# Optimization experiments

Measured on AMD Instinct MI355X. Metric: run time of the kernel, lower is better.

The kernel has to match this reference:

```python
import jax, jax.numpy as jnp
import numpy as np

DIM = 512
HEADS = 16
WS = (4, 8, 8)           # window size (z, y, x)
B = 128                  # batch * num_windows
CPB_HIDDEN = 512


def _rel_tables(ws):
    # Faithful to the torch buffers, including the original's use of ws[0]-1
    # as the normalizer for ALL three coordinate channels.
    wz, wy, wx = ws
    lz, ly, lx = 2 * wz - 1, 2 * wy - 1, 2 * wx - 1
    g = np.stack(np.meshgrid(np.arange(lz), np.arange(ly), np.arange(lx), indexing='ij'), 0).astype(np.float32)
    for i in range(3):
        g[i] = (g[i] - (wz - 1)) / (wz - 1)
    table = np.transpose(g, (1, 2, 3, 0)) * 8.0                      # [lz,ly,lx,3]
    table = np.sign(table) * np.log2(np.abs(table) + 1.0) / np.log2(8.0)
    c = np.stack(np.meshgrid(np.arange(wz), np.arange(wy), np.arange(wx), indexing='ij'), 0).reshape(3, -1)
    rel = np.transpose(c[:, :, None] - c[:, None, :], (1, 2, 0))      # [S,S,3]
    rel[:, :, 0] += wz - 1
    rel[:, :, 1] += wy - 1
    rel[:, :, 2] += wx - 1
    idx = rel[:, :, 0] * ly * lx + rel[:, :, 1] * lx + rel[:, :, 2]   # [S,S]
    return table.astype(np.float32), idx.reshape(-1).astype(np.int32)


def setup_inputs() -> dict:
    key = jax.random.key(0)
    ks = jax.random.split(key, 8)
    table, idx = _rel_tables(WS)
    return {
        'hidden_states': jax.random.normal(ks[0], (B, WS[0], WS[1], WS[2], DIM), dtype=jnp.float32),
        'Wqkv': jax.random.normal(ks[1], (3 * DIM, DIM), dtype=jnp.float32) * 0.02,
        'bqkv': jnp.zeros((3 * DIM,), dtype=jnp.float32),
        'Wproj': jax.random.normal(ks[2], (DIM, DIM), dtype=jnp.float32) * 0.02,
        'bproj': jnp.zeros((DIM,), dtype=jnp.float32),
        'logit_scale': jnp.log(10.0 * jnp.ones((HEADS, 1, 1), dtype=jnp.float32)),
        'cpb_w1': jax.random.normal(ks[3], (CPB_HIDDEN, 3), dtype=jnp.float32) * 0.02,
        'cpb_b1': jnp.zeros((CPB_HIDDEN,), dtype=jnp.float32),
        'cpb_w2': jax.random.normal(ks[4], (HEADS, CPB_HIDDEN), dtype=jnp.float32) * 0.02,
        'coords_table': jnp.asarray(table),
        'rel_index': jnp.asarray(idx),
    }


def reference(hidden_states, Wqkv, bqkv, Wproj, bproj, logit_scale,
              cpb_w1, cpb_b1, cpb_w2, coords_table, rel_index):
    b, nz, ny, nx, dim = hidden_states.shape
    H = logit_scale.shape[0]
    d = dim // H
    S = nz * ny * nx

    # qkv projection, split into per-head q/k/v: [b,H,S,d]
    qkv = hidden_states @ Wqkv.T + bqkv            # [b,nz,ny,nx,3*dim]
    qkv = qkv.reshape(b, S, 3, H, d)
    q = jnp.transpose(qkv[:, :, 0], (0, 2, 1, 3))
    k = jnp.transpose(qkv[:, :, 1], (0, 2, 1, 3))
    v = jnp.transpose(qkv[:, :, 2], (0, 2, 1, 3))

    # cosine attention: L2-normalize q,k (eps=1e-12 like F.normalize), learned clamped scale
    scale = jnp.exp(jnp.minimum(logit_scale, jnp.log(100.0)))   # [H,1,1], max 1/0.01
    qn = q / jnp.maximum(jnp.linalg.norm(q, axis=-1, keepdims=True), 1e-12)
    kn = k / jnp.maximum(jnp.linalg.norm(k, axis=-1, keepdims=True), 1e-12)
    qn = qn * scale                                              # broadcast over [b,H,S,d]

    # continuous relative position bias: MLP(coords_table) gathered by rel_index
    bias_table = jax.nn.relu(coords_table @ cpb_w1.T + cpb_b1) @ cpb_w2.T   # [lz,ly,lx,H]
    bias = bias_table.reshape(-1, H)[rel_index].reshape(S, S, H)
    bias = 16.0 * jax.nn.sigmoid(jnp.transpose(bias, (2, 0, 1)))            # [H,S,S]

    attn = jnp.einsum('bhid,bhjd->bhij', qn, kn) + bias[None]
    attn = jax.nn.softmax(attn, axis=-1)
    ctx = jnp.einsum('bhij,bhjd->bhid', attn, v)                            # [b,H,S,d]
    ctx = jnp.transpose(ctx, (0, 2, 1, 3)).reshape(b, nz, ny, nx, dim)
    return ctx @ Wproj.T + bproj
```

## Files before the change

### kernel.cpp

```cpp
#include <hip/hip_runtime.h>
#include <hip/hip_bf16.h>

typedef __bf16 bf16x8 __attribute__((ext_vector_type(8)));
typedef float  f32x4  __attribute__((ext_vector_type(4)));

#define MFMA_BF16 __builtin_amdgcn_mfma_f32_16x16x32_bf16

static __device__ __forceinline__ bf16x8 pack8(float4 a, float4 b) {
    bf16x8 r;
    r[0] = (__bf16)a.x; r[1] = (__bf16)a.y; r[2] = (__bf16)a.z; r[3] = (__bf16)a.w;
    r[4] = (__bf16)b.x; r[5] = (__bf16)b.y; r[6] = (__bf16)b.z; r[7] = (__bf16)b.w;
    return r;
}

static __device__ __forceinline__ void gload16(const void* g, void* l) {
    __builtin_amdgcn_global_load_lds(
        (const __attribute__((address_space(1))) unsigned int*)g,
        (__attribute__((address_space(3))) unsigned int*)l,
        16, 0, 0);
}

__global__ __launch_bounds__(256) void cvt_bf16_kernel(
    const float* __restrict__ src, __bf16* __restrict__ dst)
{
    const size_t i = ((size_t)blockIdx.x * 256 + threadIdx.x) * 8;
    float4 a = *(const float4*)(src + i);
    float4 b = *(const float4*)(src + i + 4);
    *(bf16x8*)(dst + i) = pack8(a, b);
}

__global__ __launch_bounds__(256) void qkv_kernel(
    const __bf16* __restrict__ hsb, const __bf16* __restrict__ Wqb,
    const float* __restrict__ bqkv, const float* __restrict__ lsc,
    __bf16* __restrict__ qn, __bf16* __restrict__ kn, __bf16* __restrict__ vv)
{
    __shared__ __align__(16) __bf16 As[128][64];
    __shared__ __align__(16) __bf16 Bs[128][64];

    const int t = threadIdx.x;
    const int nBase = blockIdx.x * 128;
    const int mBase = blockIdx.y * 128;
    const int wave = t >> 6, lane = t & 63;
    const int wr = wave >> 1, wc = wave & 1;
    const int lhi = lane >> 4, llo = lane & 15;
    const int srow = t >> 3;
    const int scol = (t & 7) * 8;

    const __bf16* gA = hsb + (size_t)(mBase + srow) * 512 + scol;
    const __bf16* gB = Wqb + (size_t)(nBase + srow) * 512 + scol;
    char* lA = (char*)(&As[0][0]) + wave * 1024;
    char* lB = (char*)(&Bs[0][0]) + wave * 1024;

    f32x4 acc[4][4] = {};

    for (int k0 = 0; k0 < 512; k0 += 64) {
        __syncthreads();
        #pragma unroll
        for (int i = 0; i < 4; ++i) {
            gload16(gA + k0 + i * 16384, lA + i * 4096);
            gload16(gB + k0 + i * 16384, lB + i * 4096);
        }
        __syncthreads();
        #pragma unroll
        for (int kk = 0; kk < 64; kk += 32) {
            bf16x8 af[4], bg[4];
            #pragma unroll
            for (int x = 0; x < 4; ++x) {
                af[x] = *(const bf16x8*)&As[wr*64 + x*16 + llo][kk + lhi*8];
                bg[x] = *(const bf16x8*)&Bs[wc*64 + x*16 + llo][kk + lhi*8];
            }
            #pragma unroll
            for (int mi = 0; mi < 4; ++mi)
                #pragma unroll
                for (int ni = 0; ni < 4; ++ni)
                    acc[mi][ni] = MFMA_BF16(af[mi], bg[ni], acc[mi][ni], 0, 0, 0);
        }
    }

    const int nW = nBase + wc * 64;
    const int which = nW >> 9;
    __bf16* outp = (which == 0) ? qn : (which == 1) ? kn : vv;
    float bq[4];
    #pragma unroll
    for (int ni = 0; ni < 4; ++ni) bq[ni] = bqkv[nW + ni*16 + llo];

    #pragma unroll
    for (int p = 0; p < 2; ++p) {
        const int h = ((nW + p*32) >> 5) & 15;
        const float sc = (which == 0) ? __expf(fminf(lsc[h], 4.6051701859880914f))
                                      : 1.0f;
        #pragma unroll
        for (int mi = 0; mi < 4; ++mi) {
            #pragma unroll
            for (int r = 0; r < 4; ++r) {
                float v0 = acc[mi][2*p][r]   + bq[2*p];
                float v1 = acc[mi][2*p+1][r] + bq[2*p+1];
                float f = 1.0f;
                if (which < 2) {
                    float ss = v0*v0 + v1*v1;
                    ss += __shfl_xor(ss, 1);
                    ss += __shfl_xor(ss, 2);
                    ss += __shfl_xor(ss, 4);
                    ss += __shfl_xor(ss, 8);
                    f = sc / fmaxf(sqrtf(ss), 1e-12f);
                }
                const int row = mBase + wr*64 + mi*16 + lhi*4 + r;
                const int b = row >> 8, s = row & 255;
                __bf16* dst = outp + (((size_t)(b*16 + h))*256 + s)*32;
                dst[llo]      = (__bf16)(v0 * f);
                dst[16 + llo] = (__bf16)(v1 * f);
            }
        }
    }
}

__global__ __launch_bounds__(256) void cpb_table_kernel(
    const float* __restrict__ w1, const float* __restrict__ b1,
    const float* __restrict__ w2, const float* __restrict__ coords,
    float* __restrict__ bias_table)
{
    __shared__ float hid[512];
    __shared__ float part[16][17];
    const int e = blockIdx.x;
    const float x = coords[e*3+0], y = coords[e*3+1], z = coords[e*3+2];
    const int t = threadIdx.x;
    for (int c = t; c < 512; c += 256) {
        float v = w1[c*3+0]*x + w1[c*3+1]*y + w1[c*3+2]*z + b1[c];
        hid[c] = fmaxf(v, 0.f);
    }
    __syncthreads();
    const int hh = t >> 4, seg = t & 15;
    float p = 0.f;
    #pragma unroll
    for (int j = 0; j < 32; ++j) p += w2[hh*512 + seg*32 + j] * hid[seg*32 + j];
    part[hh][seg] = p;
    __syncthreads();
    if (t < 16) {
        float s = 0.f;
        #pragma unroll
        for (int i = 0; i < 16; ++i) s += part[t][i];
        bias_table[e*16 + t] = s;
    }
}

__global__ __launch_bounds__(256) void bias_gather_kernel(
    const float* __restrict__ bias_table, const int* __restrict__ rel_index,
    float* __restrict__ bias_f)
{
    const int tid = blockIdx.x * 256 + threadIdx.x;
    const int lane = tid & 63;
    const int j16 = (tid >> 6) & 15;
    const int i16 = (tid >> 10) & 15;
    const int h   = tid >> 14;
    const int llo = lane & 15, lhi = lane >> 4;
    const int qrow = i16*16 + llo;
    float4 o;
    #pragma unroll
    for (int r = 0; r < 4; ++r) {
        int kcol = j16*16 + lhi*4 + r;
        int idx = rel_index[qrow*256 + kcol];
        float v = bias_table[idx*16 + h];
        (&o.x)[r] = 16.f / (1.f + __expf(-v)) - 26.0f;
    }
    ((float4*)bias_f)[tid] = o;
}

__global__ __launch_bounds__(256) void attn_kernel(
    const __bf16* __restrict__ qn, const __bf16* __restrict__ kn,
    const __bf16* __restrict__ vv, const float* __restrict__ bias_f,
    __bf16* __restrict__ ctx)
{
    __shared__ __align__(16) __bf16 Kl[256][40];
    __shared__ __align__(16) __bf16 Vt[32][264];

    const int bh = blockIdx.x;
    const int b = bh >> 4, h = bh & 15;
    const int t = threadIdx.x;
    const int wave = t >> 6, lane = t & 63;
    const int lhi = lane >> 4, llo = lane & 15;
    const size_t base = (size_t)bh * 8192;

    {
        const __bf16* sk = kn + base + t*32;
        #pragma unroll
        for (int j = 0; j < 4; ++j)
            *(bf16x8*)&Kl[t][j*8] = *(const bf16x8*)(sk + j*8);

        const int u = t & 31;
        const int slot = (t & ~31) + 8*((u & 15) >> 2) + (u & 3) + ((u >> 4) & 1)*4;
        const __bf16* sv = vv + base + t*32;
        #pragma unroll
        for (int j = 0; j < 4; ++j) {
            bf16x8 v8 = *(const bf16x8*)(sv + j*8);
            #pragma unroll
            for (int e = 0; e < 8; ++e) Vt[j*8 + e][slot] = v8[e];
        }
    }
    __syncthreads();

    const f32x4* bp4 = (const f32x4*)bias_f + (size_t)h * 16384;

    #pragma unroll 1
    for (int qt = 0; qt < 4; ++qt) {
        const int i16 = wave*4 + qt;
        const int row0 = i16*16;
        bf16x8 bq = *(const bf16x8*)(qn + base + (size_t)(row0 + llo)*32 + lhi*8);

        f32x4 o0 = {0.f,0.f,0.f,0.f}, o1 = {0.f,0.f,0.f,0.f};
        float sum = 0.f;

        #pragma unroll 2
        for (int c = 0; c < 8; ++c) {
            f32x4 bfA = bp4[((size_t)i16*16 + 2*c    )*64 + lane];
            f32x4 bfB = bp4[((size_t)i16*16 + 2*c + 1)*64 + lane];

            bf16x8 ka0 = *(const bf16x8*)&Kl[c*32 + llo][lhi*8];
            bf16x8 ka1 = *(const bf16x8*)&Kl[c*32 + 16 + llo][lhi*8];

            __builtin_amdgcn_s_setprio(1);
            f32x4 stA = MFMA_BF16(ka0, bq, bfA, 0, 0, 0);
            f32x4 stB = MFMA_BF16(ka1, bq, bfB, 0, 0, 0);
            __builtin_amdgcn_s_setprio(0);

            bf16x8 pa;
            #pragma unroll
            for (int r = 0; r < 4; ++r) {
                float eA = __expf(stA[r]);
                float eB = __expf(stB[r]);
                sum += eA + eB;
                pa[r]     = (__bf16)eA;
                pa[r + 4] = (__bf16)eB;
            }

            bf16x8 bv0 = *(const bf16x8*)&Vt[llo][c*32 + lhi*8];
            bf16x8 bv1 = *(const bf16x8*)&Vt[16 + llo][c*32 + lhi*8];

            __builtin_amdgcn_s_setprio(1);
            o0 = MFMA_BF16(pa, bv0, o0, 0, 0, 0);
            o1 = MFMA_BF16(pa, bv1, o1, 0, 0, 0);
            __builtin_amdgcn_s_setprio(0);
        }

        sum += __shfl_xor(sum, 16);
        sum += __shfl_xor(sum, 32);

        #pragma unroll
        for (int r = 0; r < 4; ++r) {
            float inv = __builtin_amdgcn_rcpf(__shfl(sum, lhi*4 + r));
            int srow = row0 + lhi*4 + r;
            __bf16* cp = ctx + ((size_t)(b*256 + srow))*512 + h*32;
            cp[llo]      = (__bf16)(o0[r] * inv);
            cp[16 + llo] = (__bf16)(o1[r] * inv);
        }
    }
}

__global__ __launch_bounds__(256) void proj_kernel(
    const __bf16* __restrict__ ctx, const __bf16* __restrict__ Wpb,
    const float* __restrict__ bpr, float* __restrict__ out)
{
    __shared__ __align__(16) __bf16 As[128][64];
    __shared__ __align__(16) __bf16 Bs[128][64];

    const int t = threadIdx.x;
    const int nBase = blockIdx.x * 128;
    const int mBase = blockIdx.y * 128;
    const int wave = t >> 6, lane = t & 63;
    const int wr = wave >> 1, wc = wave & 1;
    const int lhi = lane >> 4, llo = lane & 15;
    const int srow = t >> 3;
    const int scol = (t & 7) * 8;

    const __bf16* gA = ctx + (size_t)(mBase + srow) * 512 + scol;
    const __bf16* gB = Wpb + (size_t)(nBase + srow) * 512 + scol;
    char* lA = (char*)(&As[0][0]) + wave * 1024;
    char* lB = (char*)(&Bs[0][0]) + wave * 1024;

    f32x4 acc[4][4] = {};

    for (int k0 = 0; k0 < 512; k0 += 64) {
        __syncthreads();
        #pragma unroll
        for (int i = 0; i < 4; ++i) {
            gload16(gA + k0 + i * 16384, lA + i * 4096);
            gload16(gB + k0 + i * 16384, lB + i * 4096);
        }
        __syncthreads();
        #pragma unroll
        for (int kk = 0; kk < 64; kk += 32) {
            bf16x8 af[4], bg[4];
            #pragma unroll
            for (int x = 0; x < 4; ++x) {
                af[x] = *(const bf16x8*)&As[wr*64 + x*16 + llo][kk + lhi*8];
                bg[x] = *(const bf16x8*)&Bs[wc*64 + x*16 + llo][kk + lhi*8];
            }
            #pragma unroll
            for (int mi = 0; mi < 4; ++mi)
                #pragma unroll
                for (int ni = 0; ni < 4; ++ni)
                    acc[mi][ni] = MFMA_BF16(af[mi], bg[ni], acc[mi][ni], 0, 0, 0);
        }
    }

    float bn[4];
    #pragma unroll
    for (int ni = 0; ni < 4; ++ni) bn[ni] = bpr[nBase + wc*64 + ni*16 + llo];

    #pragma unroll
    for (int mi = 0; mi < 4; ++mi)
        #pragma unroll
        for (int ni = 0; ni < 4; ++ni)
            #pragma unroll
            for (int r = 0; r < 4; ++r)
                out[(size_t)(mBase + wr*64 + mi*16 + lhi*4 + r)*512
                    + nBase + wc*64 + ni*16 + llo] = acc[mi][ni][r] + bn[ni];
}

extern "C" void kernel_launch(void* const* d_in, const int* in_sizes, int n_in,
                              void* d_out, int out_size, void* d_ws, size_t ws_size,
                              hipStream_t stream) {
    const float* hs     = (const float*)d_in[0];
    const float* Wqkv   = (const float*)d_in[1];
    const float* bqkv   = (const float*)d_in[2];
    const float* Wproj  = (const float*)d_in[3];
    const float* bproj  = (const float*)d_in[4];
    const float* lsc    = (const float*)d_in[5];
    const float* cpb_w1 = (const float*)d_in[6];
    const float* cpb_b1 = (const float*)d_in[7];
    const float* cpb_w2 = (const float*)d_in[8];
    const float* coords = (const float*)d_in[9];
    const int*   relidx = (const int*)d_in[10];
    float* out = (float*)d_out;

    char* ws = (char*)d_ws;
    __bf16* qn     = (__bf16*)(ws);
    __bf16* kn     = (__bf16*)(ws + 33554432);
    __bf16* vv     = (__bf16*)(ws + 67108864);
    __bf16* hsb    = (__bf16*)(ws + 100663296);
    __bf16* ctx    = (__bf16*)(ws + 100663296);
    float*  bt     = (float*)(ws + 134217728);
    float*  bias_f = (float*)(ws + 134318528);
    __bf16* Wqb    = (__bf16*)(ws + 138512832);
    __bf16* Wpb    = (__bf16*)(ws + 140085696);

    cvt_bf16_kernel<<<8192, 256, 0, stream>>>(hs, hsb);
    cvt_bf16_kernel<<<384, 256, 0, stream>>>(Wqkv, Wqb);
    cvt_bf16_kernel<<<128, 256, 0, stream>>>(Wproj, Wpb);
    qkv_kernel<<<dim3(12, 256), 256, 0, stream>>>(hsb, Wqb, bqkv, lsc, qn, kn, vv);
    cpb_table_kernel<<<1575, 256, 0, stream>>>(cpb_w1, cpb_b1, cpb_w2, coords, bt);
    bias_gather_kernel<<<1024, 256, 0, stream>>>(bt, relidx, bias_f);
    attn_kernel<<<2048, 256, 0, stream>>>(qn, kn, vv, bias_f, ctx);
    proj_kernel<<<dim3(4, 256), 256, 0, stream>>>(ctx, Wpb, bproj, out);
}
```

Before: 362.9 us.

## Transpose QKV GEMM output layout for vectorized stores and swizzle block order

```diff
diff --git a/kernel.cpp b/kernel.cpp
--- a/kernel.cpp
+++ b/kernel.cpp
@@ -2,6 +2,7 @@
 #include <hip/hip_bf16.h>
 
 typedef __bf16 bf16x8 __attribute__((ext_vector_type(8)));
+typedef __bf16 bf16x4 __attribute__((ext_vector_type(4)));
 typedef float  f32x4  __attribute__((ext_vector_type(4)));
 
 #define MFMA_BF16 __builtin_amdgcn_mfma_f32_16x16x32_bf16
@@ -37,9 +38,14 @@
     __shared__ __align__(16) __bf16 As[128][64];
     __shared__ __align__(16) __bf16 Bs[128][64];
 
+    const int bid = blockIdx.x;
+    const int swz = (bid & 7) * 384 + (bid >> 3);
+    const int tileM = swz / 12;
+    const int tileN = swz - tileM * 12;
+    const int nBase = tileN * 128;
+    const int mBase = tileM * 128;
+
     const int t = threadIdx.x;
-    const int nBase = blockIdx.x * 128;
-    const int mBase = blockIdx.y * 128;
     const int wave = t >> 6, lane = t & 63;
     const int wr = wave >> 1, wc = wave & 1;
     const int lhi = lane >> 4, llo = lane & 15;
@@ -66,23 +72,25 @@
             bf16x8 af[4], bg[4];
             #pragma unroll
             for (int x = 0; x < 4; ++x) {
-                af[x] = *(const bf16x8*)&As[wr*64 + x*16 + llo][kk + lhi*8];
-                bg[x] = *(const bf16x8*)&Bs[wc*64 + x*16 + llo][kk + lhi*8];
-            }
-            #pragma unroll
-            for (int mi = 0; mi < 4; ++mi)
+                af[x] = *(const bf16x8*)&Bs[wr*64 + x*16 + llo][kk + lhi*8];
+                bg[x] = *(const bf16x8*)&As[wc*64 + x*16 + llo][kk + lhi*8];
+            }
+            #pragma unroll
+            for (int i = 0; i < 4; ++i)
                 #pragma unroll
-                for (int ni = 0; ni < 4; ++ni)
-                    acc[mi][ni] = MFMA_BF16(af[mi], bg[ni], acc[mi][ni], 0, 0, 0);
-        }
-    }
-
-    const int nW = nBase + wc * 64;
+                for (int j = 0; j < 4; ++j)
+                    acc[i][j] = MFMA_BF16(af[i], bg[j], acc[i][j], 0, 0, 0);
+        }
+    }
+
+    const int nW = nBase + wr * 64;
     const int which = nW >> 9;
     __bf16* outp = (which == 0) ? qn : (which == 1) ? kn : vv;
-    float bq[4];
-    #pragma unroll
-    for (int ni = 0; ni < 4; ++ni) bq[ni] = bqkv[nW + ni*16 + llo];
+
+    float4 bq4[4];
+    #pragma unroll
+    for (int i = 0; i < 4; ++i)
+        bq4[i] = *(const float4*)&bqkv[nW + i*16 + lhi*4];
 
     #pragma unroll
     for (int p = 0; p < 2; ++p) {
@@ -90,25 +98,41 @@
         const float sc = (which == 0) ? __expf(fminf(lsc[h], 4.6051701859880914f))
                                       : 1.0f;
         #pragma unroll
-        for (int mi = 0; mi < 4; ++mi) {
+        for (int j = 0; j < 4; ++j) {
+            float v0[4], v1[4];
+            float ss = 0.f;
             #pragma unroll
             for (int r = 0; r < 4; ++r) {
-                float v0 = acc[mi][2*p][r]   + bq[2*p];
-                float v1 = acc[mi][2*p+1][r] + bq[2*p+1];
-                float f = 1.0f;
-                if (which < 2) {
-                    float ss = v0*v0 + v1*v1;
-                    ss += __shfl_xor(ss, 1);
-                    ss += __shfl_xor(ss, 2);
-                    ss += __shfl_xor(ss, 4);
-                    ss += __shfl_xor(ss, 8);
-                    f = sc / fmaxf(sqrtf(ss), 1e-12f);
+                v0[r] = acc[2*p][j][r]   + ((const float*)&bq4[2*p])[r];
+                v1[r] = acc[2*p+1][j][r] + ((const float*)&bq4[2*p+1])[r];
+                ss += v0[r]*v0[r] + v1[r]*v1[r];
+            }
+            float f = 1.0f;
+            if (which < 2) {
+                ss += __shfl_xor(ss, 16);
+                ss += __shfl_xor(ss, 32);
+                f = sc / fmaxf(sqrtf(ss), 1e-12f);
+            }
+            const int m = mBase + wc*64 + j*16 + llo;
+            const int b = m >> 8, s = m & 255;
+            __bf16* dst = outp + ((size_t)(b*16 + h)*256 + s)*32;
+            if (which < 2) {
+                bf16x8 o;
+                #pragma unroll
+                for (int r = 0; r < 4; ++r) {
+                    o[r]     = (__bf16)(v0[r] * f);
+                    o[r + 4] = (__bf16)(v1[r] * f);
                 }
-                const int row = mBase + wr*64 + mi*16 + lhi*4 + r;
-                const int b = row >> 8, s = row & 255;
-                __bf16* dst = outp + (((size_t)(b*16 + h))*256 + s)*32;
-                dst[llo]      = (__bf16)(v0 * f);
-                dst[16 + llo] = (__bf16)(v1 * f);
+                *(bf16x8*)(dst + lhi*8) = o;
+            } else {
+                bf16x4 oa, ob;
+                #pragma unroll
+                for (int r = 0; r < 4; ++r) {
+                    oa[r] = (__bf16)v0[r];
+                    ob[r] = (__bf16)v1[r];
+                }
+                *(bf16x4*)(dst + lhi*4)      = oa;
+                *(bf16x4*)(dst + 16 + lhi*4) = ob;
             }
         }
     }
@@ -262,9 +286,12 @@
     __shared__ __align__(16) __bf16 As[128][64];
     __shared__ __align__(16) __bf16 Bs[128][64];
 
+    const int bid = blockIdx.x;
+    const int swz = (bid & 7) * 128 + (bid >> 3);
+    const int nBase = (swz & 3) * 128;
+    const int mBase = (swz >> 2) * 128;
+
     const int t = threadIdx.x;
-    const int nBase = blockIdx.x * 128;
-    const int mBase = blockIdx.y * 128;
     const int wave = t >> 6, lane = t & 63;
     const int wr = wave >> 1, wc = wave & 1;
     const int lhi = lane >> 4, llo = lane & 15;
@@ -346,9 +373,9 @@
     cvt_bf16_kernel<<<8192, 256, 0, stream>>>(hs, hsb);
     cvt_bf16_kernel<<<384, 256, 0, stream>>>(Wqkv, Wqb);
     cvt_bf16_kernel<<<128, 256, 0, stream>>>(Wproj, Wpb);
-    qkv_kernel<<<dim3(12, 256), 256, 0, stream>>>(hsb, Wqb, bqkv, lsc, qn, kn, vv);
+    qkv_kernel<<<3072, 256, 0, stream>>>(hsb, Wqb, bqkv, lsc, qn, kn, vv);
     cpb_table_kernel<<<1575, 256, 0, stream>>>(cpb_w1, cpb_b1, cpb_w2, coords, bt);
     bias_gather_kernel<<<1024, 256, 0, stream>>>(bt, relidx, bias_f);
     attn_kernel<<<2048, 256, 0, stream>>>(qn, kn, vv, bias_f, ctx);
-    proj_kernel<<<dim3(4, 256), 256, 0, stream>>>(ctx, Wpb, bproj, out);
-}
+    proj_kernel<<<1024, 256, 0, stream>>>(ctx, Wpb, bproj, out);
+}
```

After: 317.7 us. -12.5%, faster.
